# Kernel optimization log

Measured on AMD Instinct MI355X. Metric: run time of the kernel, lower is better.

## Reference

```python
import jax, jax.numpy as jnp
import numpy as np

DN = ('NCHW', 'OIHW', 'NCHW')
EPS = 1e-5


def _conv(x, w, b, stride, pad):
    y = jax.lax.conv_general_dilated(x, w, (stride, stride), ((pad, pad), (pad, pad)), dimension_numbers=DN)
    return y + b[None, :, None, None]


def _convT(x, w, b):
    # PyTorch ConvTranspose2d(k=4, s=2, p=1); w: (Cin, Cout, 4, 4)
    k = jnp.flip(w, (2, 3)).transpose(1, 0, 2, 3)  # -> (Cout, Cin, 4, 4)
    y = jax.lax.conv_general_dilated(x, k, (1, 1), ((2, 2), (2, 2)), lhs_dilation=(2, 2), dimension_numbers=DN)
    return y + b[None, :, None, None]


def _bn(x, g, b):
    # training-mode BatchNorm2d: batch stats over (N, H, W)
    m = x.mean((0, 2, 3), keepdims=True)
    v = x.var((0, 2, 3), keepdims=True)
    return (x - m) * jax.lax.rsqrt(v + EPS) * g[None, :, None, None] + b[None, :, None, None]


def _resblock(x, g1, b1, w3, b3, g2, b2, w1, b1c):
    h = jax.nn.relu(_bn(x, g1, b1))
    h = _conv(h, w3, b3, 1, 1)
    h = jax.nn.relu(_bn(h, g2, b2))
    h = _conv(h, w1, b1c, 1, 0)
    return h + x


def setup_inputs() -> dict:
    B, C, H, W, D, K = 16, 3, 128, 128, 256, 512
    key = jax.random.key(0)
    ks = iter(jax.random.split(key, 16))
    s = 0.05
    inp = {
        'x': jax.random.normal(next(ks), (B, C, H, W), jnp.float32),
        'ec1_w': jax.random.normal(next(ks), (D, C, 4, 4), jnp.float32) * s,
        'ec1_b': jnp.zeros((D,), jnp.float32),
        'ebn1_g': jnp.ones((D,), jnp.float32),
        'ebn1_b': jnp.zeros((D,), jnp.float32),
        'ec2_w': jax.random.normal(next(ks), (D, D, 4, 4), jnp.float32) * s,
        'ec2_b': jnp.zeros((D,), jnp.float32),
        # 4 residual blocks stacked: [0,1]=encoder, [2,3]=decoder
        'rb_bn1_g': jnp.ones((4, D), jnp.float32),
        'rb_bn1_b': jnp.zeros((4, D), jnp.float32),
        'rb_c3_w': jax.random.normal(next(ks), (4, D, D, 3, 3), jnp.float32) * s,
        'rb_c3_b': jnp.zeros((4, D), jnp.float32),
        'rb_bn2_g': jnp.ones((4, D), jnp.float32),
        'rb_bn2_b': jnp.zeros((4, D), jnp.float32),
        'rb_c1_w': jax.random.normal(next(ks), (4, D, D, 1, 1), jnp.float32) * s,
        'rb_c1_b': jnp.zeros((4, D), jnp.float32),
        'dbn1_g': jnp.ones((D,), jnp.float32),
        'dbn1_b': jnp.zeros((D,), jnp.float32),
        'dct1_w': jax.random.normal(next(ks), (D, D, 4, 4), jnp.float32) * s,  # (Cin, Cout, kH, kW)
        'dct1_b': jnp.zeros((D,), jnp.float32),
        'dbn2_g': jnp.ones((D,), jnp.float32),
        'dbn2_b': jnp.zeros((D,), jnp.float32),
        'dct2_w': jax.random.normal(next(ks), (D, C, 4, 4), jnp.float32) * s,
        'dct2_b': jnp.zeros((C,), jnp.float32),
        'codebook': jax.random.uniform(next(ks), (K, D), jnp.float32, -1.0 / K, 1.0 / K),
    }
    return inp


def reference(x, ec1_w, ec1_b, ebn1_g, ebn1_b, ec2_w, ec2_b,
              rb_bn1_g, rb_bn1_b, rb_c3_w, rb_c3_b, rb_bn2_g, rb_bn2_b, rb_c1_w, rb_c1_b,
              dbn1_g, dbn1_b, dct1_w, dct1_b, dbn2_g, dbn2_b, dct2_w, dct2_b, codebook):
    def rb(h, i):
        return _resblock(h, rb_bn1_g[i], rb_bn1_b[i], rb_c3_w[i], rb_c3_b[i],
                         rb_bn2_g[i], rb_bn2_b[i], rb_c1_w[i], rb_c1_b[i])

    # Encoder
    h = _conv(x, ec1_w, ec1_b, 2, 1)
    h = jax.nn.relu(_bn(h, ebn1_g, ebn1_b))
    h = _conv(h, ec2_w, ec2_b, 2, 1)
    h = rb(h, 0)
    z_e = rb(h, 1)  # [N, D, H/4, W/4]

    # Vector quantizer: argmin_k sum_d (z - w_k)^2 via norm expansion
    N, D, Hh, Ww = z_e.shape
    ze_f = z_e.transpose(0, 2, 3, 1).reshape(-1, D)  # [M, D]
    d2 = ((ze_f ** 2).sum(1, keepdims=True)
          - 2.0 * ze_f @ codebook.T
          + (codebook ** 2).sum(1)[None, :])  # [M, K]
    q = jnp.argmin(d2, axis=1)
    z_q = codebook[q].reshape(N, Hh, Ww, D).transpose(0, 3, 1, 2)

    # Decoder (takes z_e, per original forward)
    d = rb(z_e, 2)
    d = rb(d, 3)
    d = jax.nn.relu(_bn(d, dbn1_g, dbn1_b))
    d = _convT(d, dct1_w, dct1_b)
    d = jax.nn.relu(_bn(d, dbn2_g, dbn2_b))
    x_rec = _convT(d, dct2_w, dct2_b)

    return (x_rec, z_e, z_q)
```

## Files before the change

### kernel.cpp

```cpp
#include <hip/hip_runtime.h>
#include <stdint.h>

typedef __bf16 bf16_t;
typedef __bf16 bf16x8 __attribute__((ext_vector_type(8)));
typedef float f32x4 __attribute__((ext_vector_type(4)));

#define DEVINL __device__ __forceinline__

DEVINL float bf2f(bf16_t h){ return (float)h; }
DEVINL bf16_t f2bf(float f){ return (bf16_t)f; }

DEVINL void g2l16(const void* g, void* l){
  __builtin_amdgcn_global_load_lds(
      (const __attribute__((address_space(1))) uint32_t*)g,
      (__attribute__((address_space(3))) uint32_t*)l, 16, 0, 0);
}

#define SB_BYTES    9469952
#define SB0_OFF     35684352
#define STATS_OFF   73564160
#define CBN_OFF     73586688
#define WP_OFF      73588736
#define WS_NEEDED   83419136
#define WP_RB3(i) (1048576 + (i)*655360)
#define WP_RB1(i) (1048576 + (i)*655360 + 589824)
#define WP_CT     3670016
#define WP_CB     4718592
#define WP_CT2    4849664
#define WP_ELEMS  4915200

__global__ __launch_bounds__(256) void k_zero(uint4* __restrict__ p, int n16){
  int i = blockIdx.x*256 + threadIdx.x;
  if (i < n16) p[i] = make_uint4(0,0,0,0);
}

__global__ __launch_bounds__(256) void k_zerohalo(bf16_t* __restrict__ buf, int IW, int total){
  int idx = blockIdx.x*256 + threadIdx.x;
  if (idx >= total) return;
  int g8 = idx & 31, r = idx >> 5;
  int H = 4*IW - 4;
  int nn = r / H, hp = r - nn*H;
  int y, x;
  if (hp < IW){ y = 0; x = hp; }
  else if (hp < 2*IW){ y = IW-1; x = hp - IW; }
  else {
    int h2 = hp - 2*IW;
    int side = h2 / (IW-2);
    int k = h2 - side*(IW-2);
    y = k + 1; x = side ? (IW-1) : 0;
  }
  bf16_t* p = buf + ((size_t)((nn*IW + y)*IW + x))*256 + g8*8;
  bf16x8 zv;
#pragma unroll
  for (int e = 0; e < 8; e++) zv[e] = f2bf(0.f);
  *(bf16x8*)p = zv;
}

__global__ __launch_bounds__(256) void k_repack(
    const float* __restrict__ ec2_w, const float* __restrict__ rb_c3_w,
    const float* __restrict__ rb_c1_w, const float* __restrict__ dct1_w,
    const float* __restrict__ codebook, const float* __restrict__ dct2_w,
    bf16_t* __restrict__ wp)
{
  int idx = blockIdx.x*256 + threadIdx.x;
  if (idx >= WP_ELEMS) return;
  int l = idx; float v;
  if (l < 1048576) {
    int t = l>>16, co = (l>>8)&255, ci = l&255;
    v = ec2_w[co*4096 + ci*16 + t];
  } else {
    l -= 1048576;
    if (l < 2621440) {
      int i = l / 655360;
      int r = l - i*655360;
      if (r < 589824) {
        int t = r>>16, co = (r>>8)&255, ci = r&255;
        v = rb_c3_w[i*589824 + co*2304 + ci*9 + t];
      } else {
        r -= 589824;
        int co = r>>8, ci = r&255;
        v = rb_c1_w[i*65536 + co*256 + ci];
      }
    } else {
      l -= 2621440;
      if (l < 1048576) {
        int z = l>>18, r = l&262143, t = r>>16, co = (r>>8)&255, ci = r&255;
        int py = z>>1, px = z&1, a = t>>1, b = t&1;
        int ky = 2*a + 1 - py, kx = 2*b + 1 - px;
        v = dct1_w[ci*4096 + co*16 + ky*4 + kx];
      } else {
        l -= 1048576;
        if (l < 131072) {
          v = codebook[l];
        } else {
          l -= 131072;
          int z = l>>14, r = l&16383, t = r>>12, co = (r>>8)&15, ci = r&255;
          int py = z>>1, px = z&1, a = t>>1, b = t&1;
          int ky = 2*a + 1 - py, kx = 2*b + 1 - px;
          v = (co < 3) ? dct2_w[ci*48 + co*16 + ky*4 + kx] : 0.f;
        }
      }
    }
  }
  wp[idx] = f2bf(v);
}

__global__ __launch_bounds__(256) void k_cbnorm(const float* __restrict__ cb, float* __restrict__ out){
  int k = blockIdx.x*256 + threadIdx.x;
  float s = 0.f;
  for (int d = 0; d < 256; d++){ float v = cb[k*256 + d]; s += v*v; }
  out[k] = s;
}

__global__ __launch_bounds__(256) void k_convin(const float* __restrict__ x, const float* __restrict__ w,
    const float* __restrict__ bias, bf16_t* __restrict__ out)
{
  int co = threadIdx.x;
  float wr[48];
#pragma unroll
  for (int j = 0; j < 12; j++){
    float4 f = *(const float4*)(w + co*48 + j*4);
    wr[j*4+0]=f.x; wr[j*4+1]=f.y; wr[j*4+2]=f.z; wr[j*4+3]=f.w;
  }
  float bco = bias[co];
  int p0 = blockIdx.x * 16;
  for (int pi = 0; pi < 16; pi++){
    int p = p0 + pi;
    int nn = p >> 12, sp = p & 4095, oy = sp >> 6, ox = sp & 63;
    float acc = bco;
#pragma unroll
    for (int ky = 0; ky < 4; ky++){
      int iy = 2*oy + ky - 1;
      if (iy < 0 || iy > 127) continue;
#pragma unroll
      for (int kx = 0; kx < 4; kx++){
        int ix = 2*ox + kx - 1;
        if (ix < 0 || ix > 127) continue;
#pragma unroll
        for (int ci = 0; ci < 3; ci++)
          acc += x[((size_t)((nn*3+ci)*128 + iy))*128 + ix] * wr[ci*16 + ky*4 + kx];
      }
    }
    out[((size_t)((nn*66 + oy+1)*66 + ox+1))*256 + co] = f2bf(acc);
  }
}

__global__ __launch_bounds__(256) void k_bnstats(const bf16_t* __restrict__ buf, float* __restrict__ stat, int hwlog)
{
  int HW = 1 << hwlog, IW = HW + 2;
  int P = 16 << (2*hwlog);
  int tid = threadIdx.x;
  int g8 = tid & 31, ps = tid >> 5;
  float s[8], s2[8];
#pragma unroll
  for (int e = 0; e < 8; e++){ s[e] = 0.f; s2[e] = 0.f; }
  for (int p = blockIdx.x*8 + ps; p < P; p += gridDim.x*8){
    int xx = p & (HW-1), yy = (p >> hwlog) & (HW-1), nn = p >> (2*hwlog);
    bf16x8 v = *(const bf16x8*)(buf + ((size_t)((nn*IW + yy+1)*IW + xx+1))*256 + g8*8);
#pragma unroll
    for (int e = 0; e < 8; e++){ float f = bf2f(v[e]); s[e] += f; s2[e] += f*f; }
  }
  __shared__ float red[8][256];
#pragma unroll
  for (int e = 0; e < 8; e++) red[ps][g8*8+e] = s[e];
  __syncthreads();
  { float t = 0.f;
    for (int q = 0; q < 8; q++) t += red[q][tid];
    atomicAdd(&stat[tid], t); }
  __syncthreads();
#pragma unroll
  for (int e = 0; e < 8; e++) red[ps][g8*8+e] = s2[e];
  __syncthreads();
  { float t = 0.f;
    for (int q = 0; q < 8; q++) t += red[q][tid];
    atomicAdd(&stat[256 + tid], t); }
}

__global__ __launch_bounds__(256) void k_bnapply(const bf16_t* __restrict__ in, bf16_t* __restrict__ out,
    const float* __restrict__ stat, const float* __restrict__ g, const float* __restrict__ b,
    int hwlog, float invc)
{
  int idx = blockIdx.x*256 + threadIdx.x;
  int g8 = idx & 31, p = idx >> 5;
  int HW = 1 << hwlog, IW = HW + 2;
  int xx = p & (HW-1), yy = (p >> hwlog) & (HW-1), nn = p >> (2*hwlog);
  size_t a = ((size_t)((nn*IW + yy+1)*IW + xx+1))*256 + g8*8;
  float4 sm0 = *(const float4*)(stat + g8*8),     sm1 = *(const float4*)(stat + g8*8 + 4);
  float4 sq0 = *(const float4*)(stat + 256 + g8*8), sq1 = *(const float4*)(stat + 256 + g8*8 + 4);
  float4 gg0 = *(const float4*)(g + g8*8),        gg1 = *(const float4*)(g + g8*8 + 4);
  float4 bb0 = *(const float4*)(b + g8*8),        bb1 = *(const float4*)(b + g8*8 + 4);
  float sm[8] = {sm0.x,sm0.y,sm0.z,sm0.w, sm1.x,sm1.y,sm1.z,sm1.w};
  float sq[8] = {sq0.x,sq0.y,sq0.z,sq0.w, sq1.x,sq1.y,sq1.z,sq1.w};
  float gv[8] = {gg0.x,gg0.y,gg0.z,gg0.w, gg1.x,gg1.y,gg1.z,gg1.w};
  float bv[8] = {bb0.x,bb0.y,bb0.z,bb0.w, bb1.x,bb1.y,bb1.z,bb1.w};
  bf16x8 v = *(const bf16x8*)(in + a);
  bf16x8 o;
#pragma unroll
  for (int e = 0; e < 8; e++){
    float mean = sm[e]*invc;
    float var  = sq[e]*invc - mean*mean;
    float sc = gv[e] * rsqrtf(var + 1e-5f);
    float sh = bv[e] - mean*sc;
    o[e] = f2bf(fmaxf(bf2f(v[e])*sc + sh, 0.f));
  }
  *(bf16x8*)(out + a) = o;
}

template<int MODE>
__global__ __launch_bounds__(256) void k_gemm(
    const bf16_t* __restrict__ in, const bf16_t* __restrict__ wp,
    const float* __restrict__ bias, const bf16_t* __restrict__ res,
    bf16_t* __restrict__ outb, float* __restrict__ outf,
    int out_mode, float alpha)
{
  constexpr int TAPS = (MODE==0)?16:(MODE==1)?9:(MODE==2)?1:4;
  constexpr int TN   = (MODE==4)?16:64;
  constexpr int MI   = (MODE==4)?2:4;
  constexpr int MJ   = (MODE==4)?1:2;
  const int N = gridDim.y * TN;

  __shared__ __align__(16) bf16_t As[128*32];
  __shared__ __align__(16) bf16_t Bs[TN*32];

  const int tid  = threadIdx.x;
  const int lane = tid & 63;
  const int wave = tid >> 6;
  const int m0   = blockIdx.x * 128;
  const int n0   = blockIdx.y * TN;
  int py = 0, px = 0;
  const bf16_t* wpp = wp;
  if (MODE == 3){ py = blockIdx.z >> 1; px = blockIdx.z & 1; wpp += (size_t)blockIdx.z * 262144; }
  if (MODE == 4){ py = blockIdx.z >> 1; px = blockIdx.z & 1; wpp += (size_t)blockIdx.z * 16384; }

  int abase[2];
#pragma unroll
  for (int j = 0; j < 2; j++){
    int s = wave*128 + j*64 + lane;
    int ml = s >> 2, k8 = (s & 3) * 8;
    int m = m0 + ml;
    int pbase;
    if (MODE == 0){ int nn=m>>10, sp=m&1023, oy=sp>>5, ox=sp&31; pbase = (nn*66 + 2*oy)*66 + 2*ox; }
    else if (MODE == 3){ int nn=m>>10, sp=m&1023, oy=sp>>5, ox=sp&31; pbase = (nn*34 + oy+1+py)*34 + ox+1+px; }
    else if (MODE == 4){ int nn=m>>12, oyh=(m>>6)&63, oxh=m&63; pbase = (nn*66 + oyh+1+py)*66 + oxh+1+px; }
    else { int nn=m>>10, sp=m&1023, oy=sp>>5, ox=sp&31; pbase = (nn*34 + oy)*34 + ox; }
    abase[j] = pbase*256 + k8;
  }
  int bbase;
  {
    int s = (TN == 64) ? (wave*64 + lane) : lane;
    int ml = s >> 2, k8 = (s & 3) * 8;
    bbase = (n0 + ml)*256 + k8;
  }

  f32x4 acc[MI][MJ];
#pragma unroll
  for (int i = 0; i < MI; i++)
#pragma unroll
    for (int j = 0; j < MJ; j++) acc[i][j] = (f32x4){0.f,0.f,0.f,0.f};

  const int rowbase = (TN == 64) ? (wave >> 1)*64 : wave*32;
  const int colbase = (TN == 64) ? (wave & 1)*32 : 0;
  const int mf = lane & 15;
  const int kq = lane >> 4;

  for (int chunk = 0; chunk < TAPS*8; ++chunk){
    int t   = chunk >> 3;
    int ci0 = (chunk & 7) * 32;
    int toff;
    if (MODE == 0)      toff = (t >> 2)*66 + (t & 3);
    else if (MODE == 1){ int ky = t/3; toff = ky*34 + (t - ky*3); }
    else if (MODE == 2) toff = 35;
    else if (MODE == 3) toff = -((t >> 1)*34 + (t & 1));
    else                toff = -((t >> 1)*66 + (t & 1));
#pragma unroll
    for (int j = 0; j < 2; j++)
      g2l16(in + abase[j] + toff*256 + ci0, As + (wave*128 + j*64)*8);
    if (TN == 64)
      g2l16(wpp + (size_t)t*N*256 + bbase + ci0, Bs + wave*64*8);
    else if (wave == 0)
      g2l16(wpp + (size_t)t*N*256 + bbase + ci0, Bs);
    __syncthreads();

    bf16x8 af[MI], bfr[MJ];
#pragma unroll
    for (int i = 0; i < MI; i++)
      af[i]  = *reinterpret_cast<const bf16x8*>(&As[(rowbase + i*16 + mf)*32 + kq*8]);
#pragma unroll
    for (int j = 0; j < MJ; j++)
      bfr[j] = *reinterpret_cast<const bf16x8*>(&Bs[(colbase + j*16 + mf)*32 + kq*8]);
#pragma unroll
    for (int i = 0; i < MI; i++)
#pragma unroll
      for (int j = 0; j < MJ; j++)
        acc[i][j] = __builtin_amdgcn_mfma_f32_16x16x32_bf16(af[i], bfr[j], acc[i][j], 0, 0, 0);
    __syncthreads();
  }

  const int rowq = (lane >> 4) * 4;
#pragma unroll
  for (int i = 0; i < MI; i++){
#pragma unroll
    for (int r = 0; r < 4; r++){
      int m = m0 + rowbase + i*16 + rowq + r;
      if (MODE == 4){
        int nn = m >> 12, oyh = (m >> 6) & 63, oxh = m & 63;
        int co = mf;
        if (co < 3){
          float v = acc[i][0][r] + bias[co];
          outf[(size_t)nn*49152 + (size_t)co*16384 + (2*oyh+py)*128 + (2*oxh+px)] = v;
        }
      } else {
        int nn = m >> 10, sp = m & 1023, oy = sp >> 5, ox = sp & 31;
#pragma unroll
        for (int j = 0; j < MJ; j++){
          int co = n0 + colbase + j*16 + mf;
          float v = alpha * acc[i][j][r] + bias[co];
          if (res) v += bf2f(res[((size_t)((nn*34 + oy+1)*34 + ox+1))*256 + co]);
          if (out_mode == 2){
            outf[(size_t)m * N + co] = v;
          } else if (MODE == 3){
            outb[((size_t)((nn*66 + 2*oy+py+1)*66 + 2*ox+px+1))*256 + co] = f2bf(v);
          } else {
            outb[((size_t)((nn*34 + oy+1)*34 + ox+1))*256 + co] = f2bf(v);
            if (out_mode == 1)
              outf[(size_t)nn*262144 + (size_t)co*1024 + oy*32 + ox] = v;
          }
        }
      }
    }
  }
}

__global__ __launch_bounds__(256) void k_vq_argmin(const float* __restrict__ scores,
    const float* __restrict__ cb, float* __restrict__ zq)
{
  __shared__ int best[32];
  __shared__ float Z[32*256];
  int tid = threadIdx.x, lane = tid & 63, wave = tid >> 6;
  int m0 = blockIdx.x * 32;
  int nn = m0 >> 10, y = (m0 >> 5) & 31;
  for (int rr = wave; rr < 32; rr += 4){
    const float* srow = scores + (size_t)(m0 + rr) * 512;
    float bv = 3.4e38f; int bk = 0;
    for (int k = lane; k < 512; k += 64){
      float v = srow[k];
      if (v < bv){ bv = v; bk = k; }
    }
    for (int off = 32; off; off >>= 1){
      float ov = __shfl_down(bv, off);
      int   ok = __shfl_down(bk, off);
      if (ov < bv || (ov == bv && ok < bk)){ bv = ov; bk = ok; }
    }
    if (lane == 0) best[rr] = bk;
  }
  __syncthreads();
  for (int rr = 0; rr < 32; rr++)
    Z[rr*256 + tid] = cb[best[rr]*256 + tid];
  __syncthreads();
  float* orow = zq + (size_t)nn*262144 + (size_t)tid*1024 + y*32;
#pragma unroll
  for (int x4 = 0; x4 < 8; x4++){
    float4 v;
    v.x = Z[(x4*4+0)*256 + tid];
    v.y = Z[(x4*4+1)*256 + tid];
    v.z = Z[(x4*4+2)*256 + tid];
    v.w = Z[(x4*4+3)*256 + tid];
    *(float4*)(orow + x4*4) = v;
  }
}

extern "C" void kernel_launch(void* const* d_in, const int* in_sizes, int n_in,
                              void* d_out, int out_size, void* d_ws, size_t ws_size,
                              hipStream_t stream)
{
  if (ws_size < (size_t)WS_NEEDED) return;

  const float* x       = (const float*)d_in[0];
  const float* ec1_w   = (const float*)d_in[1];
  const float* ec1_b   = (const float*)d_in[2];
  const float* ebn1_g  = (const float*)d_in[3];
  const float* ebn1_b  = (const float*)d_in[4];
  const float* ec2_w   = (const float*)d_in[5];
  const float* ec2_b   = (const float*)d_in[6];
  const float* rb_bn1_g= (const float*)d_in[7];
  const float* rb_bn1_b= (const float*)d_in[8];
  const float* rb_c3_w = (const float*)d_in[9];
  const float* rb_c3_b = (const float*)d_in[10];
  const float* rb_bn2_g= (const float*)d_in[11];
  const float* rb_bn2_b= (const float*)d_in[12];
  const float* rb_c1_w = (const float*)d_in[13];
  const float* rb_c1_b = (const float*)d_in[14];
  const float* dbn1_g  = (const float*)d_in[15];
  const float* dbn1_b  = (const float*)d_in[16];
  const float* dct1_w  = (const float*)d_in[17];
  const float* dct1_b  = (const float*)d_in[18];
  const float* dbn2_g  = (const float*)d_in[19];
  const float* dbn2_b  = (const float*)d_in[20];
  const float* dct2_w  = (const float*)d_in[21];
  const float* dct2_b  = (const float*)d_in[22];
  const float* codebook= (const float*)d_in[23];

  char* ws = (char*)d_ws;
  bf16_t* A64 = (bf16_t*)ws;
  float*  scores = (float*)ws;
  bf16_t* SB0 = (bf16_t*)(ws + SB0_OFF);
  bf16_t* SB1 = (bf16_t*)(ws + SB0_OFF + 1*SB_BYTES);
  bf16_t* SB2 = (bf16_t*)(ws + SB0_OFF + 2*SB_BYTES);
  bf16_t* SB3 = (bf16_t*)(ws + SB0_OFF + 3*SB_BYTES);
  float*  stats = (float*)(ws + STATS_OFF);
  float*  cbn   = (float*)(ws + CBN_OFF);
  bf16_t* Wp    = (bf16_t*)(ws + WP_OFF);

  float* xrec = (float*)d_out;
  float* zef  = xrec + 786432;
  float* zqf  = zef + 4194304;

  k_zerohalo<<<dim3(521), 256, 0, stream>>>(A64, 66, 133120);
  k_zerohalo<<<dim3(264), 256, 0, stream>>>(SB0, 34, 67584);
  k_zerohalo<<<dim3(264), 256, 0, stream>>>(SB1, 34, 67584);
  k_zerohalo<<<dim3(264), 256, 0, stream>>>(SB2, 34, 67584);
  k_zerohalo<<<dim3(264), 256, 0, stream>>>(SB3, 34, 67584);
  k_zero  <<<dim3(6),     256, 0, stream>>>((uint4*)(ws + STATS_OFF), 1408);
  k_repack<<<dim3(19200), 256, 0, stream>>>(ec2_w, rb_c3_w, rb_c1_w, dct1_w, codebook, dct2_w, Wp);
  k_cbnorm<<<dim3(2),     256, 0, stream>>>(codebook, cbn);

  k_convin <<<dim3(4096), 256, 0, stream>>>(x, ec1_w, ec1_b, A64);
  k_bnstats<<<dim3(128),  256, 0, stream>>>(A64, stats, 6);
  k_bnapply<<<dim3(8192), 256, 0, stream>>>(A64, A64, stats, ebn1_g, ebn1_b, 6, 1.f/65536.f);
  k_gemm<0><<<dim3(128,4,1), 256, 0, stream>>>(A64, Wp, ec2_b, nullptr, SB0, nullptr, 0, 1.f);

  auto launch_rb = [&](bf16_t* xin, bf16_t* xout, int i, int sA, int sB, float* zf){
    k_bnstats<<<dim3(128),  256, 0, stream>>>(xin, stats + sA*512, 5);
    k_bnapply<<<dim3(2048), 256, 0, stream>>>(xin, SB1, stats + sA*512,
                                              rb_bn1_g + i*256, rb_bn1_b + i*256, 5, 1.f/16384.f);
    k_gemm<1><<<dim3(128,4,1), 256, 0, stream>>>(SB1, Wp + WP_RB3(i), rb_c3_b + i*256,
                                                 nullptr, SB2, nullptr, 0, 1.f);
    k_bnstats<<<dim3(128),  256, 0, stream>>>(SB2, stats + sB*512, 5);
    k_bnapply<<<dim3(2048), 256, 0, stream>>>(SB2, SB2, stats + sB*512,
                                              rb_bn2_g + i*256, rb_bn2_b + i*256, 5, 1.f/16384.f);
    k_gemm<2><<<dim3(128,4,1), 256, 0, stream>>>(SB2, Wp + WP_RB1(i), rb_c1_b + i*256,
                                                 xin, xout, zf, zf ? 1 : 0, 1.f);
  };

  launch_rb(SB0, SB3, 0, 1, 2, nullptr);
  launch_rb(SB3, SB0, 1, 3, 4, zef);

  k_gemm<2><<<dim3(128,8,1), 256, 0, stream>>>(SB0, Wp + WP_CB, cbn, nullptr, nullptr, scores, 2, -2.f);
  k_vq_argmin<<<dim3(512), 256, 0, stream>>>(scores, codebook, zqf);
  k_zerohalo<<<dim3(521), 256, 0, stream>>>(A64, 66, 133120);

  launch_rb(SB0, SB3, 2, 5, 6, nullptr);
  launch_rb(SB3, SB0, 3, 7, 8, nullptr);

  k_bnstats<<<dim3(128),  256, 0, stream>>>(SB0, stats + 9*512, 5);
  k_bnapply<<<dim3(2048), 256, 0, stream>>>(SB0, SB0, stats + 9*512, dbn1_g, dbn1_b, 5, 1.f/16384.f);
  k_gemm<3><<<dim3(128,4,4), 256, 0, stream>>>(SB0, Wp + WP_CT, dct1_b, nullptr, A64, nullptr, 0, 1.f);

  k_bnstats<<<dim3(128),  256, 0, stream>>>(A64, stats + 10*512, 6);
  k_bnapply<<<dim3(8192), 256, 0, stream>>>(A64, A64, stats + 10*512, dbn2_g, dbn2_b, 6, 1.f/65536.f);
  k_gemm<4><<<dim3(512,1,4), 256, 0, stream>>>(A64, Wp + WP_CT2, dct2_b, nullptr, nullptr, xrec, 3, 1.f);
}
```

Measured before the change: 872.4 us.

## Fuse BN stats into GEMM epilogues, widen K-tile, im2col first conv, direct final convT

```diff
diff --git a/kernel.cpp b/kernel.cpp
--- a/kernel.cpp
+++ b/kernel.cpp
@@ -21,13 +21,14 @@
 #define STATS_OFF   73564160
 #define CBN_OFF     73586688
 #define WP_OFF      73588736
-#define WS_NEEDED   83419136
+#define XI_OFF      83320832
+#define WS_NEEDED   91709440
 #define WP_RB3(i) (1048576 + (i)*655360)
 #define WP_RB1(i) (1048576 + (i)*655360 + 589824)
 #define WP_CT     3670016
 #define WP_CB     4718592
-#define WP_CT2    4849664
-#define WP_ELEMS  4915200
+#define WP_EC1    4849664
+#define WP_ELEMS  4866048
 
 __global__ __launch_bounds__(256) void k_zero(uint4* __restrict__ p, int n16){
   int i = blockIdx.x*256 + threadIdx.x;
@@ -59,7 +60,7 @@
 __global__ __launch_bounds__(256) void k_repack(
     const float* __restrict__ ec2_w, const float* __restrict__ rb_c3_w,
     const float* __restrict__ rb_c1_w, const float* __restrict__ dct1_w,
-    const float* __restrict__ codebook, const float* __restrict__ dct2_w,
+    const float* __restrict__ codebook, const float* __restrict__ ec1_w,
     bf16_t* __restrict__ wp)
 {
   int idx = blockIdx.x*256 + threadIdx.x;
@@ -94,10 +95,8 @@
           v = codebook[l];
         } else {
           l -= 131072;
-          int z = l>>14, r = l&16383, t = r>>12, co = (r>>8)&15, ci = r&255;
-          int py = z>>1, px = z&1, a = t>>1, b = t&1;
-          int ky = 2*a + 1 - py, kx = 2*b + 1 - px;
-          v = (co < 3) ? dct2_w[ci*48 + co*16 + ky*4 + kx] : 0.f;
+          int co = l>>6, k = l&63;
+          v = (k < 48) ? ec1_w[co*48 + k] : 0.f;
         }
       }
     }
@@ -112,68 +111,32 @@
   out[k] = s;
 }
 
-__global__ __launch_bounds__(256) void k_convin(const float* __restrict__ x, const float* __restrict__ w,
-    const float* __restrict__ bias, bf16_t* __restrict__ out)
-{
-  int co = threadIdx.x;
-  float wr[48];
-#pragma unroll
-  for (int j = 0; j < 12; j++){
-    float4 f = *(const float4*)(w + co*48 + j*4);
-    wr[j*4+0]=f.x; wr[j*4+1]=f.y; wr[j*4+2]=f.z; wr[j*4+3]=f.w;
-  }
-  float bco = bias[co];
-  int p0 = blockIdx.x * 16;
-  for (int pi = 0; pi < 16; pi++){
-    int p = p0 + pi;
-    int nn = p >> 12, sp = p & 4095, oy = sp >> 6, ox = sp & 63;
-    float acc = bco;
+__global__ __launch_bounds__(256) void k_im2col(const float* __restrict__ x, bf16_t* __restrict__ Xi){
+  int m = blockIdx.x*256 + threadIdx.x;
+  int nn = m >> 12, oy = (m >> 6) & 63, ox = m & 63;
+  bf16_t row[64];
+#pragma unroll
+  for (int k = 48; k < 64; k++) row[k] = f2bf(0.f);
+#pragma unroll
+  for (int ci = 0; ci < 3; ci++)
 #pragma unroll
     for (int ky = 0; ky < 4; ky++){
       int iy = 2*oy + ky - 1;
-      if (iy < 0 || iy > 127) continue;
+      bool yok = (unsigned)iy < 128u;
 #pragma unroll
       for (int kx = 0; kx < 4; kx++){
         int ix = 2*ox + kx - 1;
-        if (ix < 0 || ix > 127) continue;
-#pragma unroll
-        for (int ci = 0; ci < 3; ci++)
-          acc += x[((size_t)((nn*3+ci)*128 + iy))*128 + ix] * wr[ci*16 + ky*4 + kx];
-      }
-    }
-    out[((size_t)((nn*66 + oy+1)*66 + ox+1))*256 + co] = f2bf(acc);
-  }
-}
-
-__global__ __launch_bounds__(256) void k_bnstats(const bf16_t* __restrict__ buf, float* __restrict__ stat, int hwlog)
-{
-  int HW = 1 << hwlog, IW = HW + 2;
-  int P = 16 << (2*hwlog);
-  int tid = threadIdx.x;
-  int g8 = tid & 31, ps = tid >> 5;
-  float s[8], s2[8];
-#pragma unroll
-  for (int e = 0; e < 8; e++){ s[e] = 0.f; s2[e] = 0.f; }
-  for (int p = blockIdx.x*8 + ps; p < P; p += gridDim.x*8){
-    int xx = p & (HW-1), yy = (p >> hwlog) & (HW-1), nn = p >> (2*hwlog);
-    bf16x8 v = *(const bf16x8*)(buf + ((size_t)((nn*IW + yy+1)*IW + xx+1))*256 + g8*8);
-#pragma unroll
-    for (int e = 0; e < 8; e++){ float f = bf2f(v[e]); s[e] += f; s2[e] += f*f; }
-  }
-  __shared__ float red[8][256];
-#pragma unroll
-  for (int e = 0; e < 8; e++) red[ps][g8*8+e] = s[e];
-  __syncthreads();
-  { float t = 0.f;
-    for (int q = 0; q < 8; q++) t += red[q][tid];
-    atomicAdd(&stat[tid], t); }
-  __syncthreads();
-#pragma unroll
-  for (int e = 0; e < 8; e++) red[ps][g8*8+e] = s2[e];
-  __syncthreads();
-  { float t = 0.f;
-    for (int q = 0; q < 8; q++) t += red[q][tid];
-    atomicAdd(&stat[256 + tid], t); }
+        float v = (yok && (unsigned)ix < 128u) ? x[((size_t)((nn*3+ci)*128 + iy))*128 + ix] : 0.f;
+        row[ci*16 + ky*4 + kx] = f2bf(v);
+      }
+    }
+#pragma unroll
+  for (int u = 0; u < 8; u++){
+    bf16x8 o;
+#pragma unroll
+    for (int e = 0; e < 8; e++) o[e] = row[u*8+e];
+    *(bf16x8*)(Xi + (size_t)m*64 + u*8) = o;
+  }
 }
 
 __global__ __launch_bounds__(256) void k_bnapply(const bf16_t* __restrict__ in, bf16_t* __restrict__ out,
@@ -185,14 +148,14 @@
   int HW = 1 << hwlog, IW = HW + 2;
   int xx = p & (HW-1), yy = (p >> hwlog) & (HW-1), nn = p >> (2*hwlog);
   size_t a = ((size_t)((nn*IW + yy+1)*IW + xx+1))*256 + g8*8;
-  float4 sm0 = *(const float4*)(stat + g8*8),     sm1 = *(const float4*)(stat + g8*8 + 4);
-  float4 sq0 = *(const float4*)(stat + 256 + g8*8), sq1 = *(const float4*)(stat + 256 + g8*8 + 4);
-  float4 gg0 = *(const float4*)(g + g8*8),        gg1 = *(const float4*)(g + g8*8 + 4);
-  float4 bb0 = *(const float4*)(b + g8*8),        bb1 = *(const float4*)(b + g8*8 + 4);
-  float sm[8] = {sm0.x,sm0.y,sm0.z,sm0.w, sm1.x,sm1.y,sm1.z,sm1.w};
-  float sq[8] = {sq0.x,sq0.y,sq0.z,sq0.w, sq1.x,sq1.y,sq1.z,sq1.w};
-  float gv[8] = {gg0.x,gg0.y,gg0.z,gg0.w, gg1.x,gg1.y,gg1.z,gg1.w};
-  float bv[8] = {bb0.x,bb0.y,bb0.z,bb0.w, bb1.x,bb1.y,bb1.z,bb1.w};
+  float sm[8], sq[8], gv[8], bv[8];
+#pragma unroll
+  for (int e = 0; e < 8; e += 4){
+    *(float4*)(sm+e) = *(const float4*)(stat + g8*8 + e);
+    *(float4*)(sq+e) = *(const float4*)(stat + 256 + g8*8 + e);
+    *(float4*)(gv+e) = *(const float4*)(g + g8*8 + e);
+    *(float4*)(bv+e) = *(const float4*)(b + g8*8 + e);
+  }
   bf16x8 v = *(const bf16x8*)(in + a);
   bf16x8 o;
 #pragma unroll
@@ -211,122 +174,139 @@
     const bf16_t* __restrict__ in, const bf16_t* __restrict__ wp,
     const float* __restrict__ bias, const bf16_t* __restrict__ res,
     bf16_t* __restrict__ outb, float* __restrict__ outf,
-    int out_mode, float alpha)
+    float* __restrict__ stat, int out_mode, float alpha)
 {
-  constexpr int TAPS = (MODE==0)?16:(MODE==1)?9:(MODE==2)?1:4;
-  constexpr int TN   = (MODE==4)?16:64;
-  constexpr int MI   = (MODE==4)?2:4;
-  constexpr int MJ   = (MODE==4)?1:2;
-  const int N = gridDim.y * TN;
-
-  __shared__ __align__(16) bf16_t As[128*32];
-  __shared__ __align__(16) bf16_t Bs[TN*32];
+  constexpr int TAPS = (MODE==0)?16:(MODE==1)?9:(MODE==2)?1:(MODE==3)?4:1;
+  constexpr int CHUNKS = (MODE==5)?1:TAPS*4;
+  const int N = gridDim.y * 64;
+
+  __shared__ __align__(16) bf16_t As[128*64];
+  __shared__ __align__(16) bf16_t Bs[64*64];
+  __shared__ float s_sum[64], s_sum2[64];
 
   const int tid  = threadIdx.x;
   const int lane = tid & 63;
   const int wave = tid >> 6;
   const int m0   = blockIdx.x * 128;
-  const int n0   = blockIdx.y * TN;
+  const int n0   = blockIdx.y * 64;
   int py = 0, px = 0;
   const bf16_t* wpp = wp;
   if (MODE == 3){ py = blockIdx.z >> 1; px = blockIdx.z & 1; wpp += (size_t)blockIdx.z * 262144; }
-  if (MODE == 4){ py = blockIdx.z >> 1; px = blockIdx.z & 1; wpp += (size_t)blockIdx.z * 16384; }
-
-  int abase[2];
-#pragma unroll
-  for (int j = 0; j < 2; j++){
-    int s = wave*128 + j*64 + lane;
-    int ml = s >> 2, k8 = (s & 3) * 8;
-    int m = m0 + ml;
+
+  int abase[4];
+#pragma unroll
+  for (int j = 0; j < 4; j++){
+    int s = j*256 + wave*64 + lane;
+    int row = s >> 3, ug = (s & 7) ^ (row & 7);
+    int m = m0 + row;
     int pbase;
     if (MODE == 0){ int nn=m>>10, sp=m&1023, oy=sp>>5, ox=sp&31; pbase = (nn*66 + 2*oy)*66 + 2*ox; }
     else if (MODE == 3){ int nn=m>>10, sp=m&1023, oy=sp>>5, ox=sp&31; pbase = (nn*34 + oy+1+py)*34 + ox+1+px; }
-    else if (MODE == 4){ int nn=m>>12, oyh=(m>>6)&63, oxh=m&63; pbase = (nn*66 + oyh+1+py)*66 + oxh+1+px; }
+    else if (MODE == 5){ pbase = 0; }
     else { int nn=m>>10, sp=m&1023, oy=sp>>5, ox=sp&31; pbase = (nn*34 + oy)*34 + ox; }
-    abase[j] = pbase*256 + k8;
-  }
-  int bbase;
-  {
-    int s = (TN == 64) ? (wave*64 + lane) : lane;
-    int ml = s >> 2, k8 = (s & 3) * 8;
-    bbase = (n0 + ml)*256 + k8;
-  }
-
-  f32x4 acc[MI][MJ];
-#pragma unroll
-  for (int i = 0; i < MI; i++)
-#pragma unroll
-    for (int j = 0; j < MJ; j++) acc[i][j] = (f32x4){0.f,0.f,0.f,0.f};
-
-  const int rowbase = (TN == 64) ? (wave >> 1)*64 : wave*32;
-  const int colbase = (TN == 64) ? (wave & 1)*32 : 0;
+    abase[j] = (MODE==5) ? (m*64 + ug*8) : (pbase*256 + ug*8);
+  }
+  int bbase[2];
+#pragma unroll
+  for (int j = 0; j < 2; j++){
+    int s = j*256 + wave*64 + lane;
+    int row = s >> 3, ug = (s & 7) ^ (row & 7);
+    bbase[j] = (MODE==5) ? ((n0+row)*64 + ug*8) : ((n0+row)*256 + ug*8);
+  }
+
+  f32x4 acc[4][2];
+#pragma unroll
+  for (int i = 0; i < 4; i++)
+#pragma unroll
+    for (int j = 0; j < 2; j++) acc[i][j] = (f32x4){0.f,0.f,0.f,0.f};
+
+  const int rowbase = (wave >> 1) * 64;
+  const int colbase = (wave & 1) * 32;
   const int mf = lane & 15;
   const int kq = lane >> 4;
 
-  for (int chunk = 0; chunk < TAPS*8; ++chunk){
-    int t   = chunk >> 3;
-    int ci0 = (chunk & 7) * 32;
-    int toff;
-    if (MODE == 0)      toff = (t >> 2)*66 + (t & 3);
-    else if (MODE == 1){ int ky = t/3; toff = ky*34 + (t - ky*3); }
-    else if (MODE == 2) toff = 35;
-    else if (MODE == 3) toff = -((t >> 1)*34 + (t & 1));
-    else                toff = -((t >> 1)*66 + (t & 1));
+  for (int c = 0; c < CHUNKS; ++c){
+    int t = (MODE==5) ? 0 : (c >> 2);
+    int koff;
+    if (MODE == 0)      koff = ((t >> 2)*66 + (t & 3))*256 + ((c&3)<<6);
+    else if (MODE == 1){ int ky = t/3; koff = (ky*34 + (t - ky*3))*256 + ((c&3)<<6); }
+    else if (MODE == 2) koff = 35*256 + ((c&3)<<6);
+    else if (MODE == 3) koff = -((t >> 1)*34 + (t & 1))*256 + ((c&3)<<6);
+    else                koff = 0;
+    size_t bko = (MODE==5) ? 0 : ((size_t)t*N*256 + ((c&3)<<6));
+#pragma unroll
+    for (int j = 0; j < 4; j++)
+      g2l16(in + abase[j] + koff, As + (j*256 + wave*64)*8);
 #pragma unroll
     for (int j = 0; j < 2; j++)
-      g2l16(in + abase[j] + toff*256 + ci0, As + (wave*128 + j*64)*8);
-    if (TN == 64)
-      g2l16(wpp + (size_t)t*N*256 + bbase + ci0, Bs + wave*64*8);
-    else if (wave == 0)
-      g2l16(wpp + (size_t)t*N*256 + bbase + ci0, Bs);
+      g2l16(wpp + bko + bbase[j], Bs + (j*256 + wave*64)*8);
     __syncthreads();
 
-    bf16x8 af[MI], bfr[MJ];
-#pragma unroll
-    for (int i = 0; i < MI; i++)
-      af[i]  = *reinterpret_cast<const bf16x8*>(&As[(rowbase + i*16 + mf)*32 + kq*8]);
-#pragma unroll
-    for (int j = 0; j < MJ; j++)
-      bfr[j] = *reinterpret_cast<const bf16x8*>(&Bs[(colbase + j*16 + mf)*32 + kq*8]);
-#pragma unroll
-    for (int i = 0; i < MI; i++)
-#pragma unroll
-      for (int j = 0; j < MJ; j++)
-        acc[i][j] = __builtin_amdgcn_mfma_f32_16x16x32_bf16(af[i], bfr[j], acc[i][j], 0, 0, 0);
+#pragma unroll
+    for (int kk = 0; kk < 2; kk++){
+      bf16x8 af[4], bfr[2];
+#pragma unroll
+      for (int i = 0; i < 4; i++){
+        int rr = rowbase + i*16 + mf;
+        af[i] = *reinterpret_cast<const bf16x8*>(&As[rr*64 + (((kk*4+kq) ^ (rr&7))<<3)]);
+      }
+#pragma unroll
+      for (int j = 0; j < 2; j++){
+        int rr = colbase + j*16 + mf;
+        bfr[j] = *reinterpret_cast<const bf16x8*>(&Bs[rr*64 + (((kk*4+kq) ^ (rr&7))<<3)]);
+      }
+#pragma unroll
+      for (int i = 0; i < 4; i++)
+#pragma unroll
+        for (int j = 0; j < 2; j++)
+          acc[i][j] = __builtin_amdgcn_mfma_f32_16x16x32_bf16(af[i], bfr[j], acc[i][j], 0, 0, 0);
+    }
     __syncthreads();
   }
 
+  float psum[2] = {0.f, 0.f}, psum2[2] = {0.f, 0.f};
   const int rowq = (lane >> 4) * 4;
 #pragma unroll
-  for (int i = 0; i < MI; i++){
+  for (int i = 0; i < 4; i++){
 #pragma unroll
     for (int r = 0; r < 4; r++){
       int m = m0 + rowbase + i*16 + rowq + r;
-      if (MODE == 4){
-        int nn = m >> 12, oyh = (m >> 6) & 63, oxh = m & 63;
-        int co = mf;
-        if (co < 3){
-          float v = acc[i][0][r] + bias[co];
-          outf[(size_t)nn*49152 + (size_t)co*16384 + (2*oyh+py)*128 + (2*oxh+px)] = v;
+      int nn, oy, ox;
+      if (MODE == 5){ nn = m >> 12; oy = (m >> 6) & 63; ox = m & 63; }
+      else { nn = m >> 10; oy = (m >> 5) & 31; ox = m & 31; }
+#pragma unroll
+      for (int j = 0; j < 2; j++){
+        int co = n0 + colbase + j*16 + mf;
+        float v = alpha * acc[i][j][r] + bias[co];
+        if (res) v += bf2f(res[((size_t)((nn*34 + oy+1)*34 + ox+1))*256 + co]);
+        psum[j] += v; psum2[j] += v*v;
+        if (out_mode == 2){
+          outf[(size_t)m * N + co] = v;
+        } else if (MODE == 3){
+          outb[((size_t)((nn*66 + 2*oy+py+1)*66 + 2*ox+px+1))*256 + co] = f2bf(v);
+        } else if (MODE == 5){
+          outb[((size_t)((nn*66 + oy+1)*66 + ox+1))*256 + co] = f2bf(v);
+        } else {
+          outb[((size_t)((nn*34 + oy+1)*34 + ox+1))*256 + co] = f2bf(v);
+          if (out_mode == 1)
+            outf[(size_t)nn*262144 + (size_t)co*1024 + oy*32 + ox] = v;
         }
-      } else {
-        int nn = m >> 10, sp = m & 1023, oy = sp >> 5, ox = sp & 31;
-#pragma unroll
-        for (int j = 0; j < MJ; j++){
-          int co = n0 + colbase + j*16 + mf;
-          float v = alpha * acc[i][j][r] + bias[co];
-          if (res) v += bf2f(res[((size_t)((nn*34 + oy+1)*34 + ox+1))*256 + co]);
-          if (out_mode == 2){
-            outf[(size_t)m * N + co] = v;
-          } else if (MODE == 3){
-            outb[((size_t)((nn*66 + 2*oy+py+1)*66 + 2*ox+px+1))*256 + co] = f2bf(v);
-          } else {
-            outb[((size_t)((nn*34 + oy+1)*34 + ox+1))*256 + co] = f2bf(v);
-            if (out_mode == 1)
-              outf[(size_t)nn*262144 + (size_t)co*1024 + oy*32 + ox] = v;
-          }
-        }
-      }
+      }
+    }
+  }
+  if (stat){
+    if (tid < 64){ s_sum[tid] = 0.f; s_sum2[tid] = 0.f; }
+    __syncthreads();
+#pragma unroll
+    for (int j = 0; j < 2; j++){
+      int cl = colbase + j*16 + mf;
+      atomicAdd(&s_sum[cl], psum[j]);
+      atomicAdd(&s_sum2[cl], psum2[j]);
+    }
+    __syncthreads();
+    if (tid < 64){
+      atomicAdd(&stat[n0 + tid], s_sum[tid]);
+      atomicAdd(&stat[256 + n0 + tid], s_sum2[tid]);
     }
   }
 }
@@ -367,6 +347,81 @@
     v.w = Z[(x4*4+3)*256 + tid];
     *(float4*)(orow + x4*4) = v;
   }
+}
+
+__global__ __launch_bounds__(256) void k_convt2(const bf16_t* __restrict__ A, const float* __restrict__ w,
+    const float* __restrict__ bias, const float* __restrict__ stat,
+    const float* __restrict__ g, const float* __restrict__ b, float* __restrict__ out)
+{
+  __shared__ float sc_s[256], sh_s[256];
+  int tid = threadIdx.x;
+  {
+    float mean = stat[tid] * (1.f/65536.f);
+    float var  = stat[256+tid] * (1.f/65536.f) - mean*mean;
+    float s = g[tid] * rsqrtf(var + 1e-5f);
+    sc_s[tid] = s; sh_s[tid] = b[tid] - mean*s;
+  }
+  __syncthreads();
+  int m = blockIdx.x*256 + tid;
+  int nn = m >> 12, oyh = (m >> 6) & 63, oxh = m & 63;
+  float acc[4][3];
+#pragma unroll
+  for (int p = 0; p < 4; p++)
+#pragma unroll
+    for (int co = 0; co < 3; co++) acc[p][co] = bias[co];
+
+  const bf16_t* ipp[9]; bool vv[9];
+#pragma unroll
+  for (int dy = 0; dy < 3; dy++)
+#pragma unroll
+    for (int dx = 0; dx < 3; dx++){
+      int h = oyh + dy, ww = oxh + dx;
+      vv[dy*3+dx] = (h >= 1 && h <= 64 && ww >= 1 && ww <= 64);
+      ipp[dy*3+dx] = A + ((size_t)((nn*66 + h)*66 + ww))*256;
+    }
+
+  static const int cnt_[3] = {1,2,1};
+  static const int pys_[3][2] = {{0,0},{0,1},{1,0}};
+  static const int kys_[3][2] = {{3,0},{1,2},{0,0}};
+
+  for (int c8 = 0; c8 < 32; c8++){
+    float sc[8], sh[8];
+#pragma unroll
+    for (int e = 0; e < 8; e += 4){
+      *(float4*)(sc+e) = *(const float4*)(sc_s + c8*8 + e);
+      *(float4*)(sh+e) = *(const float4*)(sh_s + c8*8 + e);
+    }
+#pragma unroll
+    for (int dy = 0; dy < 3; dy++)
+#pragma unroll
+      for (int dx = 0; dx < 3; dx++){
+        if (!vv[dy*3+dx]) continue;
+        bf16x8 hv = *reinterpret_cast<const bf16x8*>(ipp[dy*3+dx] + c8*8);
+#pragma unroll
+        for (int e = 0; e < 8; e++){
+          int ci = c8*8 + e;
+          float f = fmaxf(bf2f(hv[e])*sc[e] + sh[e], 0.f);
+#pragma unroll
+          for (int iy = 0; iy < cnt_[dy]; iy++){
+            int py = pys_[dy][iy], ky = kys_[dy][iy];
+#pragma unroll
+            for (int ix = 0; ix < cnt_[dx]; ix++){
+              int px = pys_[dx][ix], kx = kys_[dx][ix];
+#pragma unroll
+              for (int co = 0; co < 3; co++)
+                acc[py*2+px][co] += f * w[ci*48 + co*16 + ky*4 + kx];
+            }
+          }
+        }
+      }
+  }
+#pragma unroll
+  for (int py = 0; py < 2; py++)
+#pragma unroll
+    for (int px = 0; px < 2; px++)
+#pragma unroll
+      for (int co = 0; co < 3; co++)
+        out[(size_t)nn*49152 + (size_t)co*16384 + (size_t)(2*oyh+py)*128 + (2*oxh+px)] = acc[py*2+px][co];
 }
 
 extern "C" void kernel_launch(void* const* d_in, const int* in_sizes, int n_in,
@@ -410,6 +465,7 @@
   float*  stats = (float*)(ws + STATS_OFF);
   float*  cbn   = (float*)(ws + CBN_OFF);
   bf16_t* Wp    = (bf16_t*)(ws + WP_OFF);
+  bf16_t* Xi    = (bf16_t*)(ws + XI_OFF);
 
   float* xrec = (float*)d_out;
   float* zef  = xrec + 786432;
@@ -421,42 +477,41 @@
   k_zerohalo<<<dim3(264), 256, 0, stream>>>(SB2, 34, 67584);
   k_zerohalo<<<dim3(264), 256, 0, stream>>>(SB3, 34, 67584);
   k_zero  <<<dim3(6),     256, 0, stream>>>((uint4*)(ws + STATS_OFF), 1408);
-  k_repack<<<dim3(19200), 256, 0, stream>>>(ec2_w, rb_c3_w, rb_c1_w, dct1_w, codebook, dct2_w, Wp);
+  k_repack<<<dim3(19008), 256, 0, stream>>>(ec2_w, rb_c3_w, rb_c1_w, dct1_w, codebook, ec1_w, Wp);
   k_cbnorm<<<dim3(2),     256, 0, stream>>>(codebook, cbn);
 
-  k_convin <<<dim3(4096), 256, 0, stream>>>(x, ec1_w, ec1_b, A64);
-  k_bnstats<<<dim3(128),  256, 0, stream>>>(A64, stats, 6);
+  k_im2col<<<dim3(256), 256, 0, stream>>>(x, Xi);
+  k_gemm<5><<<dim3(512,4,1), 256, 0, stream>>>(Xi, Wp + WP_EC1, ec1_b, nullptr, A64, nullptr,
+                                               stats, 0, 1.f);
   k_bnapply<<<dim3(8192), 256, 0, stream>>>(A64, A64, stats, ebn1_g, ebn1_b, 6, 1.f/65536.f);
-  k_gemm<0><<<dim3(128,4,1), 256, 0, stream>>>(A64, Wp, ec2_b, nullptr, SB0, nullptr, 0, 1.f);
-
-  auto launch_rb = [&](bf16_t* xin, bf16_t* xout, int i, int sA, int sB, float* zf){
-    k_bnstats<<<dim3(128),  256, 0, stream>>>(xin, stats + sA*512, 5);
-    k_bnapply<<<dim3(2048), 256, 0, stream>>>(xin, SB1, stats + sA*512,
+  k_gemm<0><<<dim3(128,4,1), 256, 0, stream>>>(A64, Wp, ec2_b, nullptr, SB0, nullptr,
+                                               stats + 1*512, 0, 1.f);
+
+  auto launch_rb = [&](bf16_t* xin, bf16_t* xout, int i, int sIn, int sMid, int sOut, float* zf){
+    k_bnapply<<<dim3(2048), 256, 0, stream>>>(xin, SB1, stats + sIn*512,
                                               rb_bn1_g + i*256, rb_bn1_b + i*256, 5, 1.f/16384.f);
     k_gemm<1><<<dim3(128,4,1), 256, 0, stream>>>(SB1, Wp + WP_RB3(i), rb_c3_b + i*256,
-                                                 nullptr, SB2, nullptr, 0, 1.f);
-    k_bnstats<<<dim3(128),  256, 0, stream>>>(SB2, stats + sB*512, 5);
-    k_bnapply<<<dim3(2048), 256, 0, stream>>>(SB2, SB2, stats + sB*512,
+                                                 nullptr, SB2, nullptr, stats + sMid*512, 0, 1.f);
+    k_bnapply<<<dim3(2048), 256, 0, stream>>>(SB2, SB2, stats + sMid*512,
                                               rb_bn2_g + i*256, rb_bn2_b + i*256, 5, 1.f/16384.f);
     k_gemm<2><<<dim3(128,4,1), 256, 0, stream>>>(SB2, Wp + WP_RB1(i), rb_c1_b + i*256,
-                                                 xin, xout, zf, zf ? 1 : 0, 1.f);
+                                                 xin, xout, zf, stats + sOut*512, zf ? 1 : 0, 1.f);
   };
 
-  launch_rb(SB0, SB3, 0, 1, 2, nullptr);
-  launch_rb(SB3, SB0, 1, 3, 4, zef);
-
-  k_gemm<2><<<dim3(128,8,1), 256, 0, stream>>>(SB0, Wp + WP_CB, cbn, nullptr, nullptr, scores, 2, -2.f);
+  launch_rb(SB0, SB3, 0, 1, 2, 3, nullptr);
+  launch_rb(SB3, SB0, 1, 3, 4, 5, zef);
+
+  k_gemm<2><<<dim3(128,8,1), 256, 0, stream>>>(SB0, Wp + WP_CB, cbn, nullptr, nullptr, scores,
+                                               nullptr, 2, -2.f);
   k_vq_argmin<<<dim3(512), 256, 0, stream>>>(scores, codebook, zqf);
   k_zerohalo<<<dim3(521), 256, 0, stream>>>(A64, 66, 133120);
 
-  launch_rb(SB0, SB3, 2, 5, 6, nullptr);
-  launch_rb(SB3, SB0, 3, 7, 8, nullptr);
-
-  k_bnstats<<<dim3(128),  256, 0, stream>>>(SB0, stats + 9*512, 5);
+  launch_rb(SB0, SB3, 2, 5, 6, 7, nullptr);
+  launch_rb(SB3, SB0, 3, 7, 8, 9, nullptr);
+
   k_bnapply<<<dim3(2048), 256, 0, stream>>>(SB0, SB0, stats + 9*512, dbn1_g, dbn1_b, 5, 1.f/16384.f);
-  k_gemm<3><<<dim3(128,4,4), 256, 0, stream>>>(SB0, Wp + WP_CT, dct1_b, nullptr, A64, nullptr, 0, 1.f);
-
-  k_bnstats<<<dim3(128),  256, 0, stream>>>(A64, stats + 10*512, 6);
-  k_bnapply<<<dim3(8192), 256, 0, stream>>>(A64, A64, stats + 10*512, dbn2_g, dbn2_b, 6, 1.f/65536.f);
-  k_gemm<4><<<dim3(512,1,4), 256, 0, stream>>>(A64, Wp + WP_CT2, dct2_b, nullptr, nullptr, xrec, 3, 1.f);
-}
+  k_gemm<3><<<dim3(128,4,4), 256, 0, stream>>>(SB0, Wp + WP_CT, dct1_b, nullptr, A64, nullptr,
+                                               stats + 10*512, 0, 1.f);
+
+  k_convt2<<<dim3(256), 256, 0, stream>>>(A64, dct2_w, dct2_b, stats + 10*512, dbn2_g, dbn2_b, xrec);
+}
```

New measurement: 796.7 us. -8.7%, faster.
